# Kernel optimization log

Measured on AMD Instinct MI355X. Metric: run time of the kernel, lower is better.

Reference implementation:

```python
import jax, jax.numpy as jnp
import numpy as np

INPUT_DIM = 57
D_MODEL = 64
D_STATE = 16
D_CONV = 4
EXPAND = 2
N_LAYERS = 2
OUT_SIZE = 6
D_INNER = EXPAND * D_MODEL            # 128
DT_RANK = (D_MODEL + 15) // 16        # 4
BATCH, SEQ = 4, 4096


def setup_inputs() -> dict:
    key = jax.random.key(0)
    ks = jax.random.split(key, 12)
    s = 0.02
    nl = N_LAYERS
    x = jax.random.normal(ks[0], (BATCH, SEQ, INPUT_DIM), jnp.float32)
    w_in = jax.random.normal(ks[1], (D_MODEL, INPUT_DIM), jnp.float32) * s
    b_in = jnp.zeros((D_MODEL,), jnp.float32)
    in_proj_w = jax.random.normal(ks[2], (nl, 2 * D_INNER, D_MODEL), jnp.float32) * s
    conv_w = jax.random.normal(ks[3], (nl, D_INNER, 1, D_CONV), jnp.float32) * 0.2
    conv_b = jnp.zeros((nl, D_INNER), jnp.float32)
    x_proj_w = jax.random.normal(ks[4], (nl, DT_RANK + 2 * D_STATE, D_INNER), jnp.float32) * s
    dt_proj_w = jax.random.normal(ks[5], (nl, D_INNER, DT_RANK), jnp.float32) * 0.1
    dt_proj_b = jax.random.normal(ks[6], (nl, D_INNER), jnp.float32) * 0.1
    # S4D-real init: A[d, n] = n+1  ->  A_log = log(1..d_state)
    A_log = jnp.log(jnp.broadcast_to(
        jnp.arange(1, D_STATE + 1, dtype=jnp.float32)[None, None, :],
        (nl, D_INNER, D_STATE)))
    D_skip = jnp.ones((nl, D_INNER), jnp.float32)
    out_proj_w = jax.random.normal(ks[7], (nl, D_MODEL, D_INNER), jnp.float32) * s
    w_cls = jax.random.normal(ks[8], (OUT_SIZE, D_MODEL), jnp.float32) * s
    b_cls = jnp.zeros((OUT_SIZE,), jnp.float32)
    return {"x": x, "w_in": w_in, "b_in": b_in, "in_proj_w": in_proj_w,
            "conv_w": conv_w, "conv_b": conv_b, "x_proj_w": x_proj_w,
            "dt_proj_w": dt_proj_w, "dt_proj_b": dt_proj_b, "A_log": A_log,
            "D_skip": D_skip, "out_proj_w": out_proj_w,
            "w_cls": w_cls, "b_cls": b_cls}


def _mamba_block(h, ipw, cw, cb, xpw, dpw, dpb, Alog, Dp, opw):
    B, L, _ = h.shape
    xz = h @ ipw.T                                  # (B, L, 2*D_INNER)
    xp, z = jnp.split(xz, 2, axis=-1)
    # depthwise causal conv over time
    xc = jnp.transpose(xp, (0, 2, 1))               # (B, D_INNER, L)
    xc = jax.lax.conv_general_dilated(
        xc, cw, window_strides=(1,), padding=[(D_CONV - 1, 0)],
        dimension_numbers=("NCH", "OIH", "NCH"),
        feature_group_count=D_INNER) + cb[None, :, None]
    u = jax.nn.silu(jnp.transpose(xc, (0, 2, 1)))   # (B, L, D_INNER)
    dbl = u @ xpw.T                                 # (B, L, DT_RANK + 2*D_STATE)
    dt, Bm, Cm = jnp.split(dbl, [DT_RANK, DT_RANK + D_STATE], axis=-1)
    delta = jax.nn.softplus(dt @ dpw.T + dpb)       # (B, L, D_INNER)
    A = -jnp.exp(Alog)                              # (D_INNER, D_STATE)

    def step(hst, inp):
        u_t, d_t, B_t, C_t = inp                    # (B,Di), (B,Di), (B,N), (B,N)
        hst = jnp.exp(d_t[:, :, None] * A) * hst + \
              (d_t * u_t)[:, :, None] * B_t[:, None, :]
        y_t = jnp.einsum("bdn,bn->bd", hst, C_t)
        return hst, y_t

    h0 = jnp.zeros((B, D_INNER, D_STATE), h.dtype)
    xs = (jnp.swapaxes(u, 0, 1), jnp.swapaxes(delta, 0, 1),
          jnp.swapaxes(Bm, 0, 1), jnp.swapaxes(Cm, 0, 1))
    _, ys = jax.lax.scan(step, h0, xs)              # (L, B, D_INNER)
    y = jnp.swapaxes(ys, 0, 1) + u * Dp
    y = y * jax.nn.silu(z)
    return y @ opw.T                                # (B, L, D_MODEL)


def reference(x, w_in, b_in, in_proj_w, conv_w, conv_b, x_proj_w,
              dt_proj_w, dt_proj_b, A_log, D_skip, out_proj_w, w_cls, b_cls):
    h = x @ w_in.T + b_in                           # linear_in
    for i in range(N_LAYERS):                       # residual mamba blocks
        h = h + _mamba_block(h, in_proj_w[i], conv_w[i], conv_b[i],
                             x_proj_w[i], dt_proj_w[i], dt_proj_b[i],
                             A_log[i], D_skip[i], out_proj_w[i])
    pooled = jnp.mean(h, axis=1)                    # AdaptiveAvgPool1d(1)
    return pooled @ w_cls.T + b_cls
```

## Files before the change

kernel.cpp:

```cpp
#include <hip/hip_runtime.h>


#define NB 4
#define SL 4096
#define NC 256
#define CT 16

__device__ __forceinline__ float siluf(float x) { return x / (1.f + __expf(-x)); }
__device__ __forceinline__ float softplusf(float x) { return x > 20.f ? x : log1pf(__expf(x)); }

__global__ __launch_bounds__(256) void k_prep(const float* __restrict__ opw, float* __restrict__ opwT) {
  int i = blockIdx.x * 256 + threadIdx.x;
  int l = i >> 13;
  int rem = i & 8191;
  int d = rem >> 6, m = rem & 63;
  opwT[i] = opw[l * 8192 + m * 128 + d];
}

__global__ __launch_bounds__(256) void k_linin(const float* __restrict__ x, const float* __restrict__ w,
                                               const float* __restrict__ bias, float* __restrict__ h) {
  __shared__ __align__(16) float xs[64][60];
  __shared__ __align__(16) float ws[64][60];
  const int t = threadIdx.x;
  const int r0 = blockIdx.x * 64;
  for (int i = t; i < 64 * 57; i += 256) {
    int r = i / 57, k = i - r * 57;
    xs[r][k] = x[(r0 + r) * 57 + k];
    ws[r][k] = w[i];
  }
  for (int i = t; i < 64 * 3; i += 256) {
    int r = i / 3, j = i - r * 3;
    xs[r][57 + j] = 0.f;
    ws[r][57 + j] = 0.f;
  }
  __syncthreads();
  const int col = t & 63;
  const int rg = t >> 6;
  float wreg[15][4];
#pragma unroll
  for (int k4 = 0; k4 < 15; ++k4) {
    float4 v = *(const float4*)&ws[col][k4 * 4];
    wreg[k4][0] = v.x; wreg[k4][1] = v.y; wreg[k4][2] = v.z; wreg[k4][3] = v.w;
  }
  const float bcol = bias[col];
  for (int g = 0; g < 4; ++g) {
    const int rb = rg * 16 + g * 4;
    float acc[4] = {bcol, bcol, bcol, bcol};
#pragma unroll
    for (int k4 = 0; k4 < 15; ++k4) {
#pragma unroll
      for (int i = 0; i < 4; ++i) {
        float4 xv = *(const float4*)&xs[rb + i][k4 * 4];
        acc[i] = fmaf(xv.x, wreg[k4][0], acc[i]);
        acc[i] = fmaf(xv.y, wreg[k4][1], acc[i]);
        acc[i] = fmaf(xv.z, wreg[k4][2], acc[i]);
        acc[i] = fmaf(xv.w, wreg[k4][3], acc[i]);
      }
    }
#pragma unroll
    for (int i = 0; i < 4; ++i) h[(r0 + rb + i) * 64 + col] = acc[i];
  }
}

__global__ __launch_bounds__(256) void k_inproj(const float* __restrict__ hin, const float* __restrict__ W,
                                                float* __restrict__ xp, float* __restrict__ z) {
  __shared__ __align__(16) float ht[64][68];
  __shared__ __align__(16) float wt[64][68];
  const int t = threadIdx.x;
  const int r0 = blockIdx.x * 64;
  const int c0 = blockIdx.y * 64;
  for (int idx = t; idx < 64 * 16; idx += 256) {
    int r = idx >> 4, k4 = idx & 15;
    float4 v = *(const float4*)(hin + (r0 + r) * 64 + 4 * k4);
    ht[4 * k4 + 0][r] = v.x; ht[4 * k4 + 1][r] = v.y; ht[4 * k4 + 2][r] = v.z; ht[4 * k4 + 3][r] = v.w;
  }
  for (int idx = t; idx < 64 * 16; idx += 256) {
    int c = idx >> 4, k4 = idx & 15;
    float4 v = *(const float4*)(W + (c0 + c) * 64 + 4 * k4);
    wt[4 * k4 + 0][c] = v.x; wt[4 * k4 + 1][c] = v.y; wt[4 * k4 + 2][c] = v.z; wt[4 * k4 + 3][c] = v.w;
  }
  __syncthreads();
  const int tc = t & 15, tr = t >> 4;
  float acc[4][4] = {};
  for (int k = 0; k < 64; ++k) {
    float4 a = *(const float4*)&ht[k][4 * tr];
    float4 b = *(const float4*)&wt[k][4 * tc];
    float av[4] = {a.x, a.y, a.z, a.w};
    float bv[4] = {b.x, b.y, b.z, b.w};
#pragma unroll
    for (int i = 0; i < 4; ++i)
#pragma unroll
      for (int j = 0; j < 4; ++j) acc[i][j] = fmaf(av[i], bv[j], acc[i][j]);
  }
#pragma unroll
  for (int i = 0; i < 4; ++i) {
    int row = r0 + 4 * tr + i;
    int c = c0 + 4 * tc;
    float4 v = make_float4(acc[i][0], acc[i][1], acc[i][2], acc[i][3]);
    if (c0 < 128) *(float4*)(xp + row * 128 + c) = v;
    else          *(float4*)(z + row * 128 + (c - 128)) = v;
  }
}

__global__ __launch_bounds__(256, 3) void k_mid(const float* __restrict__ xp, const float* __restrict__ cw,
                                                const float* __restrict__ cb, const float* __restrict__ xpw,
                                                const float* __restrict__ dpw, const float* __restrict__ dpb,
                                                const float* __restrict__ Alog,
                                                float* __restrict__ u_g, float* __restrict__ dl_g,
                                                float* __restrict__ B_g, float* __restrict__ C_g,
                                                float* __restrict__ chP, float* __restrict__ chH) {
  __shared__ __align__(16) float xpsh[19][132];
  __shared__ __align__(16) float ush[16][132];
  __shared__ __align__(16) float dsh[16][132];
  __shared__ __align__(16) float wsh[36][132];
  __shared__ __align__(16) float dbl[16][40];
  __shared__ float bsh[16][16];
  __shared__ float csh[16][16];

  const int t = threadIdx.x;
  const int c = blockIdx.x;
  const int b = blockIdx.y;
  const int r0 = c * CT;
  const int grow0 = b * SL + r0;

  for (int i = t; i < 19 * 128; i += 256) {
    int r = i >> 7, d = i & 127;
    float v = 0.f;
    if (!(c == 0 && r < 3)) v = xp[(size_t)(grow0 - 3 + r) * 128 + d];
    xpsh[r][d] = v;
  }
  for (int i = t; i < 36 * 128; i += 256) {
    int cc = i >> 7, d = i & 127;
    wsh[cc][d] = xpw[cc * 128 + d];
  }
  __syncthreads();

  for (int i = t; i < 16 * 128; i += 256) {
    int r = i >> 7, d = i & 127;
    float4 cwv = *(const float4*)(cw + d * 4);
    float val = cb[d] + xpsh[r][d] * cwv.x + xpsh[r + 1][d] * cwv.y +
                xpsh[r + 2][d] * cwv.z + xpsh[r + 3][d] * cwv.w;
    float uu = siluf(val);
    ush[r][d] = uu;
    u_g[(size_t)(grow0 + r) * 128 + d] = uu;
  }
  __syncthreads();

  if (t < 144) {
    int r = t / 9, cg = t - (t / 9) * 9;
    int cc = cg * 4;
    float a0 = 0, a1 = 0, a2 = 0, a3 = 0;
#pragma unroll 8
    for (int k4 = 0; k4 < 32; ++k4) {
      float4 uu = *(const float4*)&ush[r][4 * k4];
      float4 w0 = *(const float4*)&wsh[cc + 0][4 * k4];
      float4 w1 = *(const float4*)&wsh[cc + 1][4 * k4];
      float4 w2 = *(const float4*)&wsh[cc + 2][4 * k4];
      float4 w3 = *(const float4*)&wsh[cc + 3][4 * k4];
      a0 += uu.x * w0.x + uu.y * w0.y + uu.z * w0.z + uu.w * w0.w;
      a1 += uu.x * w1.x + uu.y * w1.y + uu.z * w1.z + uu.w * w1.w;
      a2 += uu.x * w2.x + uu.y * w2.y + uu.z * w2.z + uu.w * w2.w;
      a3 += uu.x * w3.x + uu.y * w3.y + uu.z * w3.z + uu.w * w3.w;
    }
    dbl[r][cc + 0] = a0; dbl[r][cc + 1] = a1; dbl[r][cc + 2] = a2; dbl[r][cc + 3] = a3;
  }
  __syncthreads();

  for (int i = t; i < 16 * 128; i += 256) {
    int r = i >> 7, d = i & 127;
    float4 wv = *(const float4*)(dpw + d * 4);
    float acc = dpb[d] + dbl[r][0] * wv.x + dbl[r][1] * wv.y + dbl[r][2] * wv.z + dbl[r][3] * wv.w;
    float dt = softplusf(acc);
    dsh[r][d] = dt;
    dl_g[(size_t)(grow0 + r) * 128 + d] = dt;
  }
  for (int i = t; i < 16 * 32; i += 256) {
    int r = i >> 5, j = i & 31;
    float v = dbl[r][4 + j];
    if (j < 16) { bsh[r][j] = v; B_g[(grow0 + r) * 16 + j] = v; }
    else        { csh[r][j - 16] = v; C_g[(grow0 + r) * 16 + (j - 16)] = v; }
  }
  __syncthreads();

  {
    const int d = t & 127, hf = t >> 7, n0 = hf * 8;
    float a[8], hst[8];
#pragma unroll
    for (int j = 0; j < 8; ++j) {
      a[j] = -__expf(Alog[d * 16 + n0 + j]);
      hst[j] = 0.f;
    }
    float dts = 0.f;
#pragma unroll 4
    for (int tt = 0; tt < CT; ++tt) {
      float dt = dsh[tt][d];
      float du = dt * ush[tt][d];
      dts += dt;
#pragma unroll
      for (int j = 0; j < 8; ++j) {
        float e = __expf(dt * a[j]);
        hst[j] = fmaf(e, hst[j], du * bsh[tt][n0 + j]);
      }
    }
    int off = ((b * 128 + d) * NC + c) * 16 + n0;
    float p[8];
#pragma unroll
    for (int j = 0; j < 8; ++j) p[j] = __expf(dts * a[j]);
    *(float4*)(chP + off + 0) = make_float4(p[0], p[1], p[2], p[3]);
    *(float4*)(chP + off + 4) = make_float4(p[4], p[5], p[6], p[7]);
    *(float4*)(chH + off + 0) = make_float4(hst[0], hst[1], hst[2], hst[3]);
    *(float4*)(chH + off + 4) = make_float4(hst[4], hst[5], hst[6], hst[7]);
  }
}

__global__ __launch_bounds__(256) void k_scan2p(const float* __restrict__ chP, float* chH) {
  __shared__ float sP[16][16];
  __shared__ float sH[16][16];
  const int t = threadIdx.x;
  const int n = t & 15, g = t >> 4;
  const int d = blockIdx.x, b = blockIdx.y;
  const int base = ((b * 128 + d) * NC) * 16 + n;

  float Pl[16], Hl[16];
  float cp = 1.f, ch = 0.f;
#pragma unroll
  for (int i = 0; i < 16; ++i) {
    int idx = base + (g * 16 + i) * 16;
    float P = chP[idx];
    float H = chH[idx];
    Pl[i] = P; Hl[i] = H;
    ch = fmaf(P, ch, H);
    cp *= P;
  }
  sP[g][n] = cp; sH[g][n] = ch;
  __syncthreads();
#pragma unroll
  for (int s = 1; s < 16; s <<= 1) {
    float pL = 1.f, hL = 0.f;
    if (g >= s) { pL = sP[g - s][n]; hL = sH[g - s][n]; }
    __syncthreads();
    ch = fmaf(cp, hL, ch);
    cp = cp * pL;
    sP[g][n] = cp; sH[g][n] = ch;
    __syncthreads();
  }
  float carry = 0.f;
  if (g > 0) carry = sH[g - 1][n];
#pragma unroll
  for (int i = 0; i < 16; ++i) {
    int idx = base + (g * 16 + i) * 16;
    chH[idx] = carry;
    carry = fmaf(Pl[i], carry, Hl[i]);
  }
}

__global__ __launch_bounds__(256, 4) void k_back(const float* __restrict__ u_g, const float* __restrict__ dl_g,
                                                 const float* __restrict__ B_g, const float* __restrict__ C_g,
                                                 const float* __restrict__ z_g, const float* __restrict__ cin,
                                                 const float* __restrict__ Alog, const float* __restrict__ Dsk,
                                                 const float* __restrict__ opwT, float* __restrict__ h) {
  __shared__ __align__(16) float ush[16][132];
  __shared__ float bsh[16][16];
  __shared__ float csh[16][16];
  __shared__ __align__(16) char poolA[2560 * 4];
  __shared__ __align__(16) char poolB[4224 * 4];

  float* dsh  = (float*)poolA;
  float* ygsh = (float*)poolA;
  float* ysh  = (float*)poolB;
  float* psh  = (float*)poolB;

  const int t = threadIdx.x;
  const int c = blockIdx.x;
  const int b = blockIdx.y;
  const int r0 = c * CT;
  const int grow0 = b * SL + r0;

  for (int i = t; i < 16 * 128; i += 256) {
    int r = i >> 7, d = i & 127;
    ush[r][d] = u_g[(size_t)(grow0 + r) * 128 + d];
    dsh[r * 132 + d] = dl_g[(size_t)(grow0 + r) * 128 + d];
  }
  for (int i = t; i < 16 * 32; i += 256) {
    int r = i >> 5, j = i & 31;
    if (j < 16) bsh[r][j] = B_g[(grow0 + r) * 16 + j];
    else        csh[r][j - 16] = C_g[(grow0 + r) * 16 + (j - 16)];
  }
  __syncthreads();

  {
    const int d = t & 127, hf = t >> 7, n0 = hf * 8;
    float a[8], hst[8];
    int off = ((b * 128 + d) * NC + c) * 16 + n0;
    float4 h0 = *(const float4*)(cin + off + 0);
    float4 h1 = *(const float4*)(cin + off + 4);
    hst[0] = h0.x; hst[1] = h0.y; hst[2] = h0.z; hst[3] = h0.w;
    hst[4] = h1.x; hst[5] = h1.y; hst[6] = h1.z; hst[7] = h1.w;
#pragma unroll
    for (int j = 0; j < 8; ++j) a[j] = -__expf(Alog[d * 16 + n0 + j]);
#pragma unroll 4
    for (int tt = 0; tt < CT; ++tt) {
      float dt = dsh[tt * 132 + d];
      float du = dt * ush[tt][d];
      float yp = 0.f;
#pragma unroll
      for (int j = 0; j < 8; ++j) {
        float e = __expf(dt * a[j]);
        hst[j] = fmaf(e, hst[j], du * bsh[tt][n0 + j]);
        yp = fmaf(hst[j], csh[tt][n0 + j], yp);
      }
      ysh[(hf * 16 + tt) * 132 + d] = yp;
    }
  }
  __syncthreads();

  for (int i = t; i < 16 * 128; i += 256) {
    int r = i >> 7, d = i & 127;
    float y = ysh[r * 132 + d] + ysh[(16 + r) * 132 + d] + ush[r][d] * Dsk[d];
    float zv = z_g[(size_t)(grow0 + r) * 128 + d];
    ygsh[d * 20 + r] = y * siluf(zv);
  }
  __syncthreads();

  {
    const int o = t & 63, q = t >> 6;
    float wreg[32];
#pragma unroll
    for (int j = 0; j < 32; ++j) wreg[j] = opwT[(q * 32 + j) * 64 + o];
    float acc[16] = {};
#pragma unroll 8
    for (int j = 0; j < 32; ++j) {
      int dd = q * 32 + j;
      const float4* yv = (const float4*)(ygsh + dd * 20);
      float4 y0 = yv[0], y1 = yv[1], y2 = yv[2], y3 = yv[3];
      float w = wreg[j];
      acc[0]  = fmaf(y0.x, w, acc[0]);  acc[1]  = fmaf(y0.y, w, acc[1]);
      acc[2]  = fmaf(y0.z, w, acc[2]);  acc[3]  = fmaf(y0.w, w, acc[3]);
      acc[4]  = fmaf(y1.x, w, acc[4]);  acc[5]  = fmaf(y1.y, w, acc[5]);
      acc[6]  = fmaf(y1.z, w, acc[6]);  acc[7]  = fmaf(y1.w, w, acc[7]);
      acc[8]  = fmaf(y2.x, w, acc[8]);  acc[9]  = fmaf(y2.y, w, acc[9]);
      acc[10] = fmaf(y2.z, w, acc[10]); acc[11] = fmaf(y2.w, w, acc[11]);
      acc[12] = fmaf(y3.x, w, acc[12]); acc[13] = fmaf(y3.y, w, acc[13]);
      acc[14] = fmaf(y3.z, w, acc[14]); acc[15] = fmaf(y3.w, w, acc[15]);
    }
    __syncthreads();
#pragma unroll
    for (int r = 0; r < 16; ++r) psh[(q * 16 + r) * 64 + o] = acc[r];
  }
  __syncthreads();

  for (int i = t; i < 16 * 64; i += 256) {
    int r = i >> 6, o = i & 63;
    float s = psh[(0 * 16 + r) * 64 + o] + psh[(1 * 16 + r) * 64 + o] +
              psh[(2 * 16 + r) * 64 + o] + psh[(3 * 16 + r) * 64 + o];
    h[(size_t)(grow0 + r) * 64 + o] += s;
  }
}

__global__ __launch_bounds__(256) void k_poolpart(const float* __restrict__ h, float* __restrict__ pp) {
  const int lb = blockIdx.x;
  const int b = blockIdx.y;
  const int t = threadIdx.x;
  const int d = t & 63, part = t >> 6;
  float s = 0.f;
  for (int i = 0; i < 32; ++i) {
    int l = lb * 128 + part + i * 4;
    s += h[(size_t)(b * SL + l) * 64 + d];
  }
  __shared__ float red[256];
  red[t] = s;
  __syncthreads();
  if (t < 64) pp[(b * 32 + lb) * 64 + t] = red[t] + red[t + 64] + red[t + 128] + red[t + 192];
}

__global__ __launch_bounds__(256) void k_cls(const float* __restrict__ pp, const float* __restrict__ wc,
                                             const float* __restrict__ bc, float* __restrict__ out) {
  const int t = threadIdx.x;
  __shared__ float pooled[4][64];
  int b = t >> 6, d = t & 63;
  float s = 0.f;
  for (int lb = 0; lb < 32; ++lb) s += pp[(b * 32 + lb) * 64 + d];
  pooled[b][d] = s * (1.f / 4096.f);
  __syncthreads();
  if (t < 24) {
    int bb = t / 6, o = t - bb * 6;
    float acc = bc[o];
    for (int d2 = 0; d2 < 64; ++d2) acc += pooled[bb][d2] * wc[o * 64 + d2];
    out[bb * 6 + o] = acc;
  }
}

extern "C" void kernel_launch(void* const* d_in, const int* in_sizes, int n_in,
                              void* d_out, int out_size, void* d_ws, size_t ws_size,
                              hipStream_t stream) {
  const float* x    = (const float*)d_in[0];
  const float* w_in = (const float*)d_in[1];
  const float* b_in = (const float*)d_in[2];
  const float* ipw  = (const float*)d_in[3];
  const float* cw   = (const float*)d_in[4];
  const float* cb   = (const float*)d_in[5];
  const float* xpw  = (const float*)d_in[6];
  const float* dpw  = (const float*)d_in[7];
  const float* dpb  = (const float*)d_in[8];
  const float* Alog = (const float*)d_in[9];
  const float* Dsk  = (const float*)d_in[10];
  const float* opw  = (const float*)d_in[11];
  const float* wc   = (const float*)d_in[12];
  const float* bc   = (const float*)d_in[13];
  float* out = (float*)d_out;

  float* ws   = (float*)d_ws;
  float* h    = ws;
  float* xp   = h + 1048576;
  float* zb   = xp + 2097152;
  float* ub   = zb + 2097152;
  float* dl   = ub + 2097152;
  float* Bb   = dl + 2097152;
  float* Cb   = Bb + 262144;
  float* chP  = Cb + 262144;
  float* chH  = chP + 2097152;
  float* opwT = chH + 2097152;
  float* pp   = opwT + 16384;

  k_prep<<<64, 256, 0, stream>>>(opw, opwT);
  k_linin<<<256, 256, 0, stream>>>(x, w_in, b_in, h);
  for (int i = 0; i < 2; ++i) {
    k_inproj<<<dim3(256, 4), 256, 0, stream>>>(h, ipw + i * 16384, xp, zb);
    k_mid<<<dim3(NC, 4), 256, 0, stream>>>(xp, cw + i * 512, cb + i * 128,
                                           xpw + i * 4608, dpw + i * 512, dpb + i * 128,
                                           Alog + i * 2048, ub, dl, Bb, Cb, chP, chH);
    k_scan2p<<<dim3(128, 4), 256, 0, stream>>>(chP, chH);
    k_back<<<dim3(NC, 4), 256, 0, stream>>>(ub, dl, Bb, Cb, zb, chH,
                                            Alog + i * 2048, Dsk + i * 128,
                                            opwT + i * 8192, h);
  }
  k_poolpart<<<dim3(32, 4), 256, 0, stream>>>(h, pp);
  k_cls<<<1, 256, 0, stream>>>(pp, wc, bc, out);
}
```

Measured before the change: 248.8 us.

## Fuse mid, chunk scan and back kernels into one cooperative kernel

Replaces the three per-layer kernels (chunk-local scan, inter-chunk prefix scan, output pass) with a single cooperative kernel that uses grid-wide syncs. u, delta, B and C stay in shared memory instead of going through global buffers, and the chunk length doubles to 32 with half as many chunks. The inter-chunk carry becomes a serial loop over 128 chunks per (b,d,n) thread, rebuilding the decay from stored dt sums, in place of the parallel tree scan. The cost is two grid barriers, a serial carry loop run by only 8192 threads, and the requirement that all 512 blocks be co-resident at two blocks per CU.

```diff
diff --git a/kernel.cpp b/kernel.cpp
--- a/kernel.cpp
+++ b/kernel.cpp
@@ -1,10 +1,13 @@
 #include <hip/hip_runtime.h>
+#include <hip/hip_cooperative_groups.h>
 
 
 #define NB 4
 #define SL 4096
-#define NC 256
-#define CT 16
+#define NC 128
+#define CT 32
+
+namespace cg = cooperative_groups;
 
 __device__ __forceinline__ float siluf(float x) { return x / (1.f + __expf(-x)); }
 __device__ __forceinline__ float softplusf(float x) { return x > 20.f ? x : log1pf(__expf(x)); }
@@ -102,61 +105,62 @@
   }
 }
 
-__global__ __launch_bounds__(256, 3) void k_mid(const float* __restrict__ xp, const float* __restrict__ cw,
-                                                const float* __restrict__ cb, const float* __restrict__ xpw,
-                                                const float* __restrict__ dpw, const float* __restrict__ dpb,
-                                                const float* __restrict__ Alog,
-                                                float* __restrict__ u_g, float* __restrict__ dl_g,
-                                                float* __restrict__ B_g, float* __restrict__ C_g,
-                                                float* __restrict__ chP, float* __restrict__ chH) {
-  __shared__ __align__(16) float xpsh[19][132];
-  __shared__ __align__(16) float ush[16][132];
-  __shared__ __align__(16) float dsh[16][132];
-  __shared__ __align__(16) float wsh[36][132];
-  __shared__ __align__(16) float dbl[16][40];
-  __shared__ float bsh[16][16];
-  __shared__ float csh[16][16];
+__global__ __launch_bounds__(256, 2) void k_coop(
+    const float* __restrict__ xp, const float* __restrict__ z_g,
+    const float* __restrict__ cw, const float* __restrict__ cb,
+    const float* __restrict__ xpw, const float* __restrict__ dpw, const float* __restrict__ dpb,
+    const float* __restrict__ Alog, const float* __restrict__ Dsk, const float* __restrict__ opwT,
+    float* __restrict__ summary, float* __restrict__ dtsumG, float* __restrict__ cinG,
+    float* __restrict__ h) {
+  __shared__ __align__(16) float ush[32][132];
+  __shared__ __align__(16) float dsh[32][132];
+  __shared__ __align__(16) float dbl[32][40];
+  __shared__ __align__(16) char poolX[35 * 132 * 4];
+  __shared__ __align__(16) char poolW[36 * 132 * 4];
+
+  float* xpsh = (float*)poolX;
+  float* ysh  = (float*)poolX;
+  float* wsh  = (float*)poolW;
+  float* ygsh = (float*)poolW;
 
   const int t = threadIdx.x;
   const int c = blockIdx.x;
   const int b = blockIdx.y;
-  const int r0 = c * CT;
-  const int grow0 = b * SL + r0;
-
-  for (int i = t; i < 19 * 128; i += 256) {
-    int r = i >> 7, d = i & 127;
+  const int grow0 = b * SL + c * CT;
+  const int d = t & 127, hf = t >> 7, n0 = hf * 8;
+
+  for (int i = t; i < 35 * 128; i += 256) {
+    int r = i >> 7, dd = i & 127;
     float v = 0.f;
-    if (!(c == 0 && r < 3)) v = xp[(size_t)(grow0 - 3 + r) * 128 + d];
-    xpsh[r][d] = v;
+    if (!(c == 0 && r < 3)) v = xp[(size_t)(grow0 - 3 + r) * 128 + dd];
+    xpsh[r * 132 + dd] = v;
   }
   for (int i = t; i < 36 * 128; i += 256) {
-    int cc = i >> 7, d = i & 127;
-    wsh[cc][d] = xpw[cc * 128 + d];
-  }
-  __syncthreads();
-
-  for (int i = t; i < 16 * 128; i += 256) {
-    int r = i >> 7, d = i & 127;
-    float4 cwv = *(const float4*)(cw + d * 4);
-    float val = cb[d] + xpsh[r][d] * cwv.x + xpsh[r + 1][d] * cwv.y +
-                xpsh[r + 2][d] * cwv.z + xpsh[r + 3][d] * cwv.w;
-    float uu = siluf(val);
-    ush[r][d] = uu;
-    u_g[(size_t)(grow0 + r) * 128 + d] = uu;
-  }
-  __syncthreads();
-
-  if (t < 144) {
-    int r = t / 9, cg = t - (t / 9) * 9;
-    int cc = cg * 4;
+    int cc = i >> 7, dd = i & 127;
+    wsh[cc * 132 + dd] = xpw[cc * 128 + dd];
+  }
+  __syncthreads();
+
+  for (int i = t; i < 32 * 128; i += 256) {
+    int r = i >> 7, dd = i & 127;
+    float4 cwv = *(const float4*)(cw + dd * 4);
+    float val = cb[dd] + xpsh[r * 132 + dd] * cwv.x + xpsh[(r + 1) * 132 + dd] * cwv.y +
+                xpsh[(r + 2) * 132 + dd] * cwv.z + xpsh[(r + 3) * 132 + dd] * cwv.w;
+    ush[r][dd] = siluf(val);
+  }
+  __syncthreads();
+
+  for (int idx = t; idx < 32 * 9; idx += 256) {
+    int r = idx / 9, cg2 = idx - (idx / 9) * 9;
+    int cc = cg2 * 4;
     float a0 = 0, a1 = 0, a2 = 0, a3 = 0;
 #pragma unroll 8
     for (int k4 = 0; k4 < 32; ++k4) {
       float4 uu = *(const float4*)&ush[r][4 * k4];
-      float4 w0 = *(const float4*)&wsh[cc + 0][4 * k4];
-      float4 w1 = *(const float4*)&wsh[cc + 1][4 * k4];
-      float4 w2 = *(const float4*)&wsh[cc + 2][4 * k4];
-      float4 w3 = *(const float4*)&wsh[cc + 3][4 * k4];
+      float4 w0 = *(const float4*)&wsh[(cc + 0) * 132 + 4 * k4];
+      float4 w1 = *(const float4*)&wsh[(cc + 1) * 132 + 4 * k4];
+      float4 w2 = *(const float4*)&wsh[(cc + 2) * 132 + 4 * k4];
+      float4 w3 = *(const float4*)&wsh[(cc + 3) * 132 + 4 * k4];
       a0 += uu.x * w0.x + uu.y * w0.y + uu.z * w0.z + uu.w * w0.w;
       a1 += uu.x * w1.x + uu.y * w1.y + uu.z * w1.z + uu.w * w1.w;
       a2 += uu.x * w2.x + uu.y * w2.y + uu.z * w2.z + uu.w * w2.w;
@@ -166,30 +170,19 @@
   }
   __syncthreads();
 
-  for (int i = t; i < 16 * 128; i += 256) {
-    int r = i >> 7, d = i & 127;
-    float4 wv = *(const float4*)(dpw + d * 4);
-    float acc = dpb[d] + dbl[r][0] * wv.x + dbl[r][1] * wv.y + dbl[r][2] * wv.z + dbl[r][3] * wv.w;
-    float dt = softplusf(acc);
-    dsh[r][d] = dt;
-    dl_g[(size_t)(grow0 + r) * 128 + d] = dt;
-  }
-  for (int i = t; i < 16 * 32; i += 256) {
-    int r = i >> 5, j = i & 31;
-    float v = dbl[r][4 + j];
-    if (j < 16) { bsh[r][j] = v; B_g[(grow0 + r) * 16 + j] = v; }
-    else        { csh[r][j - 16] = v; C_g[(grow0 + r) * 16 + (j - 16)] = v; }
-  }
-  __syncthreads();
-
+  for (int i = t; i < 32 * 128; i += 256) {
+    int r = i >> 7, dd = i & 127;
+    float4 wv = *(const float4*)(dpw + dd * 4);
+    float acc = dpb[dd] + dbl[r][0] * wv.x + dbl[r][1] * wv.y + dbl[r][2] * wv.z + dbl[r][3] * wv.w;
+    dsh[r][dd] = softplusf(acc);
+  }
+  __syncthreads();
+
+  float a[8];
+#pragma unroll
+  for (int j = 0; j < 8; ++j) a[j] = -__expf(Alog[d * 16 + n0 + j]);
   {
-    const int d = t & 127, hf = t >> 7, n0 = hf * 8;
-    float a[8], hst[8];
-#pragma unroll
-    for (int j = 0; j < 8; ++j) {
-      a[j] = -__expf(Alog[d * 16 + n0 + j]);
-      hst[j] = 0.f;
-    }
+    float hst[8] = {};
     float dts = 0.f;
 #pragma unroll 4
     for (int tt = 0; tt < CT; ++tt) {
@@ -199,161 +192,92 @@
 #pragma unroll
       for (int j = 0; j < 8; ++j) {
         float e = __expf(dt * a[j]);
-        hst[j] = fmaf(e, hst[j], du * bsh[tt][n0 + j]);
+        hst[j] = fmaf(e, hst[j], du * dbl[tt][4 + n0 + j]);
       }
     }
-    int off = ((b * 128 + d) * NC + c) * 16 + n0;
-    float p[8];
-#pragma unroll
-    for (int j = 0; j < 8; ++j) p[j] = __expf(dts * a[j]);
-    *(float4*)(chP + off + 0) = make_float4(p[0], p[1], p[2], p[3]);
-    *(float4*)(chP + off + 4) = make_float4(p[4], p[5], p[6], p[7]);
-    *(float4*)(chH + off + 0) = make_float4(hst[0], hst[1], hst[2], hst[3]);
-    *(float4*)(chH + off + 4) = make_float4(hst[4], hst[5], hst[6], hst[7]);
-  }
-}
-
-__global__ __launch_bounds__(256) void k_scan2p(const float* __restrict__ chP, float* chH) {
-  __shared__ float sP[16][16];
-  __shared__ float sH[16][16];
-  const int t = threadIdx.x;
-  const int n = t & 15, g = t >> 4;
-  const int d = blockIdx.x, b = blockIdx.y;
-  const int base = ((b * 128 + d) * NC) * 16 + n;
-
-  float Pl[16], Hl[16];
-  float cp = 1.f, ch = 0.f;
-#pragma unroll
-  for (int i = 0; i < 16; ++i) {
-    int idx = base + (g * 16 + i) * 16;
-    float P = chP[idx];
-    float H = chH[idx];
-    Pl[i] = P; Hl[i] = H;
-    ch = fmaf(P, ch, H);
-    cp *= P;
-  }
-  sP[g][n] = cp; sH[g][n] = ch;
-  __syncthreads();
-#pragma unroll
-  for (int s = 1; s < 16; s <<= 1) {
-    float pL = 1.f, hL = 0.f;
-    if (g >= s) { pL = sP[g - s][n]; hL = sH[g - s][n]; }
-    __syncthreads();
-    ch = fmaf(cp, hL, ch);
-    cp = cp * pL;
-    sP[g][n] = cp; sH[g][n] = ch;
-    __syncthreads();
-  }
-  float carry = 0.f;
-  if (g > 0) carry = sH[g - 1][n];
-#pragma unroll
-  for (int i = 0; i < 16; ++i) {
-    int idx = base + (g * 16 + i) * 16;
-    chH[idx] = carry;
-    carry = fmaf(Pl[i], carry, Hl[i]);
-  }
-}
-
-__global__ __launch_bounds__(256, 4) void k_back(const float* __restrict__ u_g, const float* __restrict__ dl_g,
-                                                 const float* __restrict__ B_g, const float* __restrict__ C_g,
-                                                 const float* __restrict__ z_g, const float* __restrict__ cin,
-                                                 const float* __restrict__ Alog, const float* __restrict__ Dsk,
-                                                 const float* __restrict__ opwT, float* __restrict__ h) {
-  __shared__ __align__(16) float ush[16][132];
-  __shared__ float bsh[16][16];
-  __shared__ float csh[16][16];
-  __shared__ __align__(16) char poolA[2560 * 4];
-  __shared__ __align__(16) char poolB[4224 * 4];
-
-  float* dsh  = (float*)poolA;
-  float* ygsh = (float*)poolA;
-  float* ysh  = (float*)poolB;
-  float* psh  = (float*)poolB;
-
-  const int t = threadIdx.x;
-  const int c = blockIdx.x;
-  const int b = blockIdx.y;
-  const int r0 = c * CT;
-  const int grow0 = b * SL + r0;
-
-  for (int i = t; i < 16 * 128; i += 256) {
-    int r = i >> 7, d = i & 127;
-    ush[r][d] = u_g[(size_t)(grow0 + r) * 128 + d];
-    dsh[r * 132 + d] = dl_g[(size_t)(grow0 + r) * 128 + d];
-  }
-  for (int i = t; i < 16 * 32; i += 256) {
-    int r = i >> 5, j = i & 31;
-    if (j < 16) bsh[r][j] = B_g[(grow0 + r) * 16 + j];
-    else        csh[r][j - 16] = C_g[(grow0 + r) * 16 + (j - 16)];
-  }
-  __syncthreads();
+    size_t off = ((size_t)(b * NC + c) * 128 + d) * 16 + n0;
+    *(float4*)(summary + off + 0) = make_float4(hst[0], hst[1], hst[2], hst[3]);
+    *(float4*)(summary + off + 4) = make_float4(hst[4], hst[5], hst[6], hst[7]);
+    if (hf == 0) dtsumG[(b * NC + c) * 128 + d] = dts;
+  }
+
+  cg::this_grid().sync();
 
   {
-    const int d = t & 127, hf = t >> 7, n0 = hf * 8;
-    float a[8], hst[8];
-    int off = ((b * 128 + d) * NC + c) * 16 + n0;
-    float4 h0 = *(const float4*)(cin + off + 0);
-    float4 h1 = *(const float4*)(cin + off + 4);
+    int gid = (blockIdx.y * gridDim.x + blockIdx.x) * 256 + t;
+    if (gid < NB * 128 * 16) {
+      int n2 = gid & 15, d2 = (gid >> 4) & 127, b2 = gid >> 11;
+      float A2 = -__expf(Alog[d2 * 16 + n2]);
+      float carry = 0.f;
+#pragma unroll 4
+      for (int c2 = 0; c2 < NC; ++c2) {
+        size_t base = ((size_t)(b2 * NC + c2) * 128 + d2) * 16 + n2;
+        float Hl = summary[base];
+        float ds = dtsumG[(b2 * NC + c2) * 128 + d2];
+        cinG[base] = carry;
+        carry = fmaf(__expf(ds * A2), carry, Hl);
+      }
+    }
+  }
+
+  cg::this_grid().sync();
+
+  float yp[CT];
+  {
+    float hst[8];
+    size_t off = ((size_t)(b * NC + c) * 128 + d) * 16 + n0;
+    float4 h0 = *(const float4*)(cinG + off + 0);
+    float4 h1 = *(const float4*)(cinG + off + 4);
     hst[0] = h0.x; hst[1] = h0.y; hst[2] = h0.z; hst[3] = h0.w;
     hst[4] = h1.x; hst[5] = h1.y; hst[6] = h1.z; hst[7] = h1.w;
-#pragma unroll
-    for (int j = 0; j < 8; ++j) a[j] = -__expf(Alog[d * 16 + n0 + j]);
 #pragma unroll 4
     for (int tt = 0; tt < CT; ++tt) {
-      float dt = dsh[tt * 132 + d];
+      float dt = dsh[tt][d];
       float du = dt * ush[tt][d];
-      float yp = 0.f;
+      float yv = 0.f;
 #pragma unroll
       for (int j = 0; j < 8; ++j) {
         float e = __expf(dt * a[j]);
-        hst[j] = fmaf(e, hst[j], du * bsh[tt][n0 + j]);
-        yp = fmaf(hst[j], csh[tt][n0 + j], yp);
+        hst[j] = fmaf(e, hst[j], du * dbl[tt][4 + n0 + j]);
+        yv = fmaf(hst[j], dbl[tt][20 + n0 + j], yv);
       }
-      ysh[(hf * 16 + tt) * 132 + d] = yp;
-    }
-  }
-  __syncthreads();
-
-  for (int i = t; i < 16 * 128; i += 256) {
-    int r = i >> 7, d = i & 127;
-    float y = ysh[r * 132 + d] + ysh[(16 + r) * 132 + d] + ush[r][d] * Dsk[d];
-    float zv = z_g[(size_t)(grow0 + r) * 128 + d];
-    ygsh[d * 20 + r] = y * siluf(zv);
+      yp[tt] = yv;
+    }
+  }
+  if (hf == 0) {
+#pragma unroll 4
+    for (int tt = 0; tt < CT; ++tt) ysh[tt * 132 + d] = yp[tt];
+  }
+  __syncthreads();
+  if (hf == 1) {
+#pragma unroll 4
+    for (int tt = 0; tt < CT; ++tt) ysh[tt * 132 + d] += yp[tt];
+  }
+  __syncthreads();
+
+  for (int i = t; i < 32 * 128; i += 256) {
+    int r = i >> 7, dd = i & 127;
+    float y = ysh[r * 132 + dd] + ush[r][dd] * Dsk[dd];
+    float zv = z_g[(size_t)(grow0 + r) * 128 + dd];
+    ygsh[dd * 36 + r] = y * siluf(zv);
   }
   __syncthreads();
 
   {
     const int o = t & 63, q = t >> 6;
-    float wreg[32];
-#pragma unroll
-    for (int j = 0; j < 32; ++j) wreg[j] = opwT[(q * 32 + j) * 64 + o];
-    float acc[16] = {};
-#pragma unroll 8
-    for (int j = 0; j < 32; ++j) {
-      int dd = q * 32 + j;
-      const float4* yv = (const float4*)(ygsh + dd * 20);
-      float4 y0 = yv[0], y1 = yv[1], y2 = yv[2], y3 = yv[3];
-      float w = wreg[j];
-      acc[0]  = fmaf(y0.x, w, acc[0]);  acc[1]  = fmaf(y0.y, w, acc[1]);
-      acc[2]  = fmaf(y0.z, w, acc[2]);  acc[3]  = fmaf(y0.w, w, acc[3]);
-      acc[4]  = fmaf(y1.x, w, acc[4]);  acc[5]  = fmaf(y1.y, w, acc[5]);
-      acc[6]  = fmaf(y1.z, w, acc[6]);  acc[7]  = fmaf(y1.w, w, acc[7]);
-      acc[8]  = fmaf(y2.x, w, acc[8]);  acc[9]  = fmaf(y2.y, w, acc[9]);
-      acc[10] = fmaf(y2.z, w, acc[10]); acc[11] = fmaf(y2.w, w, acc[11]);
-      acc[12] = fmaf(y3.x, w, acc[12]); acc[13] = fmaf(y3.y, w, acc[13]);
-      acc[14] = fmaf(y3.z, w, acc[14]); acc[15] = fmaf(y3.w, w, acc[15]);
-    }
-    __syncthreads();
-#pragma unroll
-    for (int r = 0; r < 16; ++r) psh[(q * 16 + r) * 64 + o] = acc[r];
-  }
-  __syncthreads();
-
-  for (int i = t; i < 16 * 64; i += 256) {
-    int r = i >> 6, o = i & 63;
-    float s = psh[(0 * 16 + r) * 64 + o] + psh[(1 * 16 + r) * 64 + o] +
-              psh[(2 * 16 + r) * 64 + o] + psh[(3 * 16 + r) * 64 + o];
-    h[(size_t)(grow0 + r) * 64 + o] += s;
+    float acc[8] = {};
+    for (int k = 0; k < 128; ++k) {
+      float w = opwT[k * 64 + o];
+      float4 y0 = *(const float4*)&ygsh[k * 36 + q * 8];
+      float4 y1 = *(const float4*)&ygsh[k * 36 + q * 8 + 4];
+      acc[0] = fmaf(y0.x, w, acc[0]); acc[1] = fmaf(y0.y, w, acc[1]);
+      acc[2] = fmaf(y0.z, w, acc[2]); acc[3] = fmaf(y0.w, w, acc[3]);
+      acc[4] = fmaf(y1.x, w, acc[4]); acc[5] = fmaf(y1.y, w, acc[5]);
+      acc[6] = fmaf(y1.z, w, acc[6]); acc[7] = fmaf(y1.w, w, acc[7]);
+    }
+#pragma unroll
+    for (int j = 0; j < 8; ++j)
+      h[(size_t)(grow0 + q * 8 + j) * 64 + o] += acc[j];
   }
 }
 
@@ -409,30 +333,35 @@
   const float* bc   = (const float*)d_in[13];
   float* out = (float*)d_out;
 
-  float* ws   = (float*)d_ws;
-  float* h    = ws;
-  float* xp   = h + 1048576;
-  float* zb   = xp + 2097152;
-  float* ub   = zb + 2097152;
-  float* dl   = ub + 2097152;
-  float* Bb   = dl + 2097152;
-  float* Cb   = Bb + 262144;
-  float* chP  = Cb + 262144;
-  float* chH  = chP + 2097152;
-  float* opwT = chH + 2097152;
-  float* pp   = opwT + 16384;
+  float* ws      = (float*)d_ws;
+  float* h       = ws;
+  float* xp      = h + 1048576;
+  float* zb      = xp + 2097152;
+  float* summary = zb + 2097152;
+  float* dtsum   = summary + 1048576;
+  float* cin     = dtsum + 65536;
+  float* opwT    = cin + 1048576;
+  float* pp      = opwT + 16384;
 
   k_prep<<<64, 256, 0, stream>>>(opw, opwT);
   k_linin<<<256, 256, 0, stream>>>(x, w_in, b_in, h);
   for (int i = 0; i < 2; ++i) {
     k_inproj<<<dim3(256, 4), 256, 0, stream>>>(h, ipw + i * 16384, xp, zb);
-    k_mid<<<dim3(NC, 4), 256, 0, stream>>>(xp, cw + i * 512, cb + i * 128,
-                                           xpw + i * 4608, dpw + i * 512, dpb + i * 128,
-                                           Alog + i * 2048, ub, dl, Bb, Cb, chP, chH);
-    k_scan2p<<<dim3(128, 4), 256, 0, stream>>>(chP, chH);
-    k_back<<<dim3(NC, 4), 256, 0, stream>>>(ub, dl, Bb, Cb, zb, chH,
-                                            Alog + i * 2048, Dsk + i * 128,
-                                            opwT + i * 8192, h);
+    const float* cwi  = cw + i * 512;
+    const float* cbi  = cb + i * 128;
+    const float* xpwi = xpw + i * 4608;
+    const float* dpwi = dpw + i * 512;
+    const float* dpbi = dpb + i * 128;
+    const float* Ali  = Alog + i * 2048;
+    const float* Dsi  = Dsk + i * 128;
+    const float* opTi = opwT + i * 8192;
+    void* coopArgs[] = {
+      (void*)&xp, (void*)&zb, (void*)&cwi, (void*)&cbi, (void*)&xpwi,
+      (void*)&dpwi, (void*)&dpbi, (void*)&Ali, (void*)&Dsi, (void*)&opTi,
+      (void*)&summary, (void*)&dtsum, (void*)&cin, (void*)&h
+    };
+    hipLaunchCooperativeKernel((const void*)k_coop, dim3(NC, NB), dim3(256),
+                               coopArgs, 0, stream);
   }
   k_poolpart<<<dim3(32, 4), 256, 0, stream>>>(h, pp);
   k_cls<<<1, 256, 0, stream>>>(pp, wc, bc, out);
```

Result: slower. 516.2 us (+107.5%).

## Trim shared memory in scan kernels and fuse output reduction via shuffles

Applied to the files above, without the earlier changes.

In k_mid, the conv input staging buffer is dropped: the causal conv now reads xp straight from global memory with boundary checks, and B is read from the dbl buffer instead of separate bsh/csh copies. This cuts LDS use so the occupancy hint can rise from 3 to 4 blocks. In k_back, each d's two state halves now sit in adjacent lanes, so y is combined with a shuffle and the gated output is written directly, removing a staging pass and a barrier. The out-projection now splits over rows instead of over k, with no cross-warp partial-sum reduction, but each weight is read from global memory 4 times more often. The occupancy hint goes from 4 to 5.

```diff
diff --git a/kernel.cpp b/kernel.cpp
--- a/kernel.cpp
+++ b/kernel.cpp
@@ -102,47 +102,39 @@
   }
 }
 
-__global__ __launch_bounds__(256, 3) void k_mid(const float* __restrict__ xp, const float* __restrict__ cw,
+__global__ __launch_bounds__(256, 4) void k_mid(const float* __restrict__ xp, const float* __restrict__ cw,
                                                 const float* __restrict__ cb, const float* __restrict__ xpw,
                                                 const float* __restrict__ dpw, const float* __restrict__ dpb,
                                                 const float* __restrict__ Alog,
                                                 float* __restrict__ u_g, float* __restrict__ dl_g,
                                                 float* __restrict__ B_g, float* __restrict__ C_g,
                                                 float* __restrict__ chP, float* __restrict__ chH) {
-  __shared__ __align__(16) float xpsh[19][132];
   __shared__ __align__(16) float ush[16][132];
   __shared__ __align__(16) float dsh[16][132];
   __shared__ __align__(16) float wsh[36][132];
   __shared__ __align__(16) float dbl[16][40];
-  __shared__ float bsh[16][16];
-  __shared__ float csh[16][16];
 
   const int t = threadIdx.x;
   const int c = blockIdx.x;
   const int b = blockIdx.y;
-  const int r0 = c * CT;
-  const int grow0 = b * SL + r0;
-
-  for (int i = t; i < 19 * 128; i += 256) {
-    int r = i >> 7, d = i & 127;
-    float v = 0.f;
-    if (!(c == 0 && r < 3)) v = xp[(size_t)(grow0 - 3 + r) * 128 + d];
-    xpsh[r][d] = v;
-  }
+  const int grow0 = b * SL + c * CT;
+
   for (int i = t; i < 36 * 128; i += 256) {
-    int cc = i >> 7, d = i & 127;
-    wsh[cc][d] = xpw[cc * 128 + d];
-  }
-  __syncthreads();
-
+    int cc = i >> 7, dd = i & 127;
+    wsh[cc][dd] = xpw[cc * 128 + dd];
+  }
   for (int i = t; i < 16 * 128; i += 256) {
-    int r = i >> 7, d = i & 127;
-    float4 cwv = *(const float4*)(cw + d * 4);
-    float val = cb[d] + xpsh[r][d] * cwv.x + xpsh[r + 1][d] * cwv.y +
-                xpsh[r + 2][d] * cwv.z + xpsh[r + 3][d] * cwv.w;
-    float uu = siluf(val);
-    ush[r][d] = uu;
-    u_g[(size_t)(grow0 + r) * 128 + d] = uu;
+    int r = i >> 7, dd = i & 127;
+    float4 cwv = *(const float4*)(cw + dd * 4);
+    const float* base = xp + (size_t)(grow0 + r) * 128 + dd;
+    int l = c * CT + r;
+    float acc = cb[dd] + base[0] * cwv.w;
+    if (l >= 1) acc += base[-128] * cwv.z;
+    if (l >= 2) acc += base[-256] * cwv.y;
+    if (l >= 3) acc += base[-384] * cwv.x;
+    float uu = siluf(acc);
+    ush[r][dd] = uu;
+    u_g[(size_t)(grow0 + r) * 128 + dd] = uu;
   }
   __syncthreads();
 
@@ -167,18 +159,18 @@
   __syncthreads();
 
   for (int i = t; i < 16 * 128; i += 256) {
-    int r = i >> 7, d = i & 127;
-    float4 wv = *(const float4*)(dpw + d * 4);
-    float acc = dpb[d] + dbl[r][0] * wv.x + dbl[r][1] * wv.y + dbl[r][2] * wv.z + dbl[r][3] * wv.w;
+    int r = i >> 7, dd = i & 127;
+    float4 wv = *(const float4*)(dpw + dd * 4);
+    float acc = dpb[dd] + dbl[r][0] * wv.x + dbl[r][1] * wv.y + dbl[r][2] * wv.z + dbl[r][3] * wv.w;
     float dt = softplusf(acc);
-    dsh[r][d] = dt;
-    dl_g[(size_t)(grow0 + r) * 128 + d] = dt;
+    dsh[r][dd] = dt;
+    dl_g[(size_t)(grow0 + r) * 128 + dd] = dt;
   }
   for (int i = t; i < 16 * 32; i += 256) {
     int r = i >> 5, j = i & 31;
     float v = dbl[r][4 + j];
-    if (j < 16) { bsh[r][j] = v; B_g[(grow0 + r) * 16 + j] = v; }
-    else        { csh[r][j - 16] = v; C_g[(grow0 + r) * 16 + (j - 16)] = v; }
+    if (j < 16) B_g[(grow0 + r) * 16 + j] = v;
+    else        C_g[(grow0 + r) * 16 + (j - 16)] = v;
   }
   __syncthreads();
 
@@ -199,7 +191,7 @@
 #pragma unroll
       for (int j = 0; j < 8; ++j) {
         float e = __expf(dt * a[j]);
-        hst[j] = fmaf(e, hst[j], du * bsh[tt][n0 + j]);
+        hst[j] = fmaf(e, hst[j], du * dbl[tt][4 + n0 + j]);
       }
     }
     int off = ((b * 128 + d) * NC + c) * 16 + n0;
@@ -254,32 +246,26 @@
   }
 }
 
-__global__ __launch_bounds__(256, 4) void k_back(const float* __restrict__ u_g, const float* __restrict__ dl_g,
+__global__ __launch_bounds__(256, 5) void k_back(const float* __restrict__ u_g, const float* __restrict__ dl_g,
                                                  const float* __restrict__ B_g, const float* __restrict__ C_g,
                                                  const float* __restrict__ z_g, const float* __restrict__ cin,
                                                  const float* __restrict__ Alog, const float* __restrict__ Dsk,
                                                  const float* __restrict__ opwT, float* __restrict__ h) {
   __shared__ __align__(16) float ush[16][132];
+  __shared__ __align__(16) float dsh[16][132];
   __shared__ float bsh[16][16];
   __shared__ float csh[16][16];
-  __shared__ __align__(16) char poolA[2560 * 4];
-  __shared__ __align__(16) char poolB[4224 * 4];
-
-  float* dsh  = (float*)poolA;
-  float* ygsh = (float*)poolA;
-  float* ysh  = (float*)poolB;
-  float* psh  = (float*)poolB;
+  __shared__ __align__(16) float ygsh[128][20];
 
   const int t = threadIdx.x;
   const int c = blockIdx.x;
   const int b = blockIdx.y;
-  const int r0 = c * CT;
-  const int grow0 = b * SL + r0;
+  const int grow0 = b * SL + c * CT;
 
   for (int i = t; i < 16 * 128; i += 256) {
-    int r = i >> 7, d = i & 127;
-    ush[r][d] = u_g[(size_t)(grow0 + r) * 128 + d];
-    dsh[r * 132 + d] = dl_g[(size_t)(grow0 + r) * 128 + d];
+    int r = i >> 7, dd = i & 127;
+    ush[r][dd] = u_g[(size_t)(grow0 + r) * 128 + dd];
+    dsh[r][dd] = dl_g[(size_t)(grow0 + r) * 128 + dd];
   }
   for (int i = t; i < 16 * 32; i += 256) {
     int r = i >> 5, j = i & 31;
@@ -289,71 +275,54 @@
   __syncthreads();
 
   {
-    const int d = t & 127, hf = t >> 7, n0 = hf * 8;
+    const int d = t >> 1, hf = t & 1, n0 = hf * 8;
     float a[8], hst[8];
-    int off = ((b * 128 + d) * NC + c) * 16 + n0;
+    size_t off = ((size_t)(b * 128 + d) * NC + c) * 16 + n0;
     float4 h0 = *(const float4*)(cin + off + 0);
     float4 h1 = *(const float4*)(cin + off + 4);
     hst[0] = h0.x; hst[1] = h0.y; hst[2] = h0.z; hst[3] = h0.w;
     hst[4] = h1.x; hst[5] = h1.y; hst[6] = h1.z; hst[7] = h1.w;
 #pragma unroll
     for (int j = 0; j < 8; ++j) a[j] = -__expf(Alog[d * 16 + n0 + j]);
+    const float Dd = Dsk[d];
 #pragma unroll 4
     for (int tt = 0; tt < CT; ++tt) {
-      float dt = dsh[tt * 132 + d];
-      float du = dt * ush[tt][d];
-      float yp = 0.f;
+      float dt = dsh[tt][d];
+      float ut = ush[tt][d];
+      float du = dt * ut;
+      float yv = 0.f;
 #pragma unroll
       for (int j = 0; j < 8; ++j) {
         float e = __expf(dt * a[j]);
         hst[j] = fmaf(e, hst[j], du * bsh[tt][n0 + j]);
-        yp = fmaf(hst[j], csh[tt][n0 + j], yp);
+        yv = fmaf(hst[j], csh[tt][n0 + j], yv);
       }
-      ysh[(hf * 16 + tt) * 132 + d] = yp;
-    }
-  }
-  __syncthreads();
-
-  for (int i = t; i < 16 * 128; i += 256) {
-    int r = i >> 7, d = i & 127;
-    float y = ysh[r * 132 + d] + ysh[(16 + r) * 132 + d] + ush[r][d] * Dsk[d];
-    float zv = z_g[(size_t)(grow0 + r) * 128 + d];
-    ygsh[d * 20 + r] = y * siluf(zv);
+      float tot = yv + __shfl_xor(yv, 1);
+      if (hf == 0) {
+        float y = tot + ut * Dd;
+        float zv = z_g[(size_t)(grow0 + tt) * 128 + d];
+        ygsh[d][tt] = y * siluf(zv);
+      }
+    }
   }
   __syncthreads();
 
   {
     const int o = t & 63, q = t >> 6;
-    float wreg[32];
-#pragma unroll
-    for (int j = 0; j < 32; ++j) wreg[j] = opwT[(q * 32 + j) * 64 + o];
-    float acc[16] = {};
+    float acc0 = 0.f, acc1 = 0.f, acc2 = 0.f, acc3 = 0.f;
 #pragma unroll 8
-    for (int j = 0; j < 32; ++j) {
-      int dd = q * 32 + j;
-      const float4* yv = (const float4*)(ygsh + dd * 20);
-      float4 y0 = yv[0], y1 = yv[1], y2 = yv[2], y3 = yv[3];
-      float w = wreg[j];
-      acc[0]  = fmaf(y0.x, w, acc[0]);  acc[1]  = fmaf(y0.y, w, acc[1]);
-      acc[2]  = fmaf(y0.z, w, acc[2]);  acc[3]  = fmaf(y0.w, w, acc[3]);
-      acc[4]  = fmaf(y1.x, w, acc[4]);  acc[5]  = fmaf(y1.y, w, acc[5]);
-      acc[6]  = fmaf(y1.z, w, acc[6]);  acc[7]  = fmaf(y1.w, w, acc[7]);
-      acc[8]  = fmaf(y2.x, w, acc[8]);  acc[9]  = fmaf(y2.y, w, acc[9]);
-      acc[10] = fmaf(y2.z, w, acc[10]); acc[11] = fmaf(y2.w, w, acc[11]);
-      acc[12] = fmaf(y3.x, w, acc[12]); acc[13] = fmaf(y3.y, w, acc[13]);
-      acc[14] = fmaf(y3.z, w, acc[14]); acc[15] = fmaf(y3.w, w, acc[15]);
-    }
-    __syncthreads();
-#pragma unroll
-    for (int r = 0; r < 16; ++r) psh[(q * 16 + r) * 64 + o] = acc[r];
-  }
-  __syncthreads();
-
-  for (int i = t; i < 16 * 64; i += 256) {
-    int r = i >> 6, o = i & 63;
-    float s = psh[(0 * 16 + r) * 64 + o] + psh[(1 * 16 + r) * 64 + o] +
-              psh[(2 * 16 + r) * 64 + o] + psh[(3 * 16 + r) * 64 + o];
-    h[(size_t)(grow0 + r) * 64 + o] += s;
+    for (int k = 0; k < 128; ++k) {
+      float w = opwT[k * 64 + o];
+      float4 yv = *(const float4*)&ygsh[k][q * 4];
+      acc0 = fmaf(yv.x, w, acc0);
+      acc1 = fmaf(yv.y, w, acc1);
+      acc2 = fmaf(yv.z, w, acc2);
+      acc3 = fmaf(yv.w, w, acc3);
+    }
+    h[(size_t)(grow0 + q * 4 + 0) * 64 + o] += acc0;
+    h[(size_t)(grow0 + q * 4 + 1) * 64 + o] += acc1;
+    h[(size_t)(grow0 + q * 4 + 2) * 64 + o] += acc2;
+    h[(size_t)(grow0 + q * 4 + 3) * 64 + o] += acc3;
   }
 }
 
```

After: 246.7 us. Within noise of the previous version (-0.8%).
